# Kernel tuning notes

Hardware: AMD Instinct MI355X
Metric: run time of the kernel (lower is better)

The kernel has to match this reference:

```python
import jax, jax.numpy as jnp
import numpy as np

S, B, H, D, G = 2048, 2, 16, 128, 16  # seq, batch, heads, head_dim, v-quant groups


def setup_inputs() -> dict:
    key = jax.random.key(0)
    ks = jax.random.split(key, 9)
    # int8-valued activations stored as float (torch code does .to(torch.int8))
    q = jax.random.randint(ks[0], (S, B, H, D), -128, 128).astype(jnp.float32)
    k = jax.random.randint(ks[1], (S, B, H, D), -128, 128).astype(jnp.float32)
    v = jax.random.randint(ks[2], (S, B, H, D), -128, 128).astype(jnp.float32)
    qmin = jax.random.normal(ks[3], (S, B, H, 1), jnp.float32) * 0.01
    qscale = jax.random.uniform(ks[4], (S, B, H, 1), jnp.float32, 0.005, 0.02)
    kmin = jax.random.normal(ks[5], (S, B, H, 1), jnp.float32) * 0.01
    kscale = jax.random.uniform(ks[6], (S, B, H, 1), jnp.float32, 0.005, 0.02)
    vmin = jax.random.normal(ks[7], (G, B, H, D, 1), jnp.float32) * 0.01
    vscale = jax.random.uniform(ks[8], (G, B, H, D, 1), jnp.float32, 0.005, 0.02)
    return {"query_layer": q, "key_layer": k, "value_layer": v,
            "qmin": qmin, "qscale": qscale, "kmin": kmin, "kscale": kscale,
            "vmin": vmin, "vscale": vscale, "causal": 1}


def _attention(query_layer, key_layer, value_layer, qmin, qscale, kmin, kscale, vmin, vscale, causal):
    # s b h d -> b h s d ; emulate .to(torch.int8) (values are already int8-range ints)
    q = jnp.transpose(query_layer, (1, 2, 0, 3))
    k = jnp.transpose(key_layer, (1, 2, 0, 3))
    v = jnp.transpose(value_layer, (1, 2, 0, 3))
    # per-token quant factors: s b h 1 -> b h s 1
    qm = jnp.transpose(qmin[..., 0], (1, 2, 0))[..., None]
    qs = jnp.transpose(qscale[..., 0], (1, 2, 0))[..., None]
    km = jnp.transpose(kmin[..., 0], (1, 2, 0))[..., None]
    ksc = jnp.transpose(kscale[..., 0], (1, 2, 0))[..., None]
    # attnq_qk: dequantize per-token then QK^T
    qd = q * qs + qm
    kd = k * ksc + km
    scores = jnp.einsum('bhsd,bhtd->bhst', qd, kd)
    # softmaxq: scale by 1/sqrt(128), causal mask, softmax, int8 requant of probs
    scores = scores * jnp.float32(1.0 / np.sqrt(128.0))
    s = scores.shape[-1]
    if causal:
        mask = jnp.tril(jnp.ones((s, s), dtype=bool))
        scores = jnp.where(mask, scores, jnp.float32(-1e9))
    probs = jax.nn.softmax(scores, axis=-1)
    pmin = jnp.min(probs, axis=-1, keepdims=True)
    pmax = jnp.max(probs, axis=-1, keepdims=True)
    pscale = (pmax - pmin) / 255.0 + jnp.float32(1e-12)
    quant_prob = jnp.round((probs - pmin) / pscale)  # int8-range prob codes
    # attnq_pv: dequant probs (per query token) and V (per sequence group) then PV
    pd = quant_prob * pscale + pmin
    vm = jnp.transpose(vmin[..., 0], (1, 2, 0, 3))  # b h g d
    vs = jnp.transpose(vscale[..., 0], (1, 2, 0, 3))
    gs = v.shape[2] // vm.shape[2]  # group size along sequence
    vd = v * jnp.repeat(vs, gs, axis=2) + jnp.repeat(vm, gs, axis=2)
    out = jnp.einsum('bhst,bhtd->bhsd', pd, vd)
    b, h, sq, d = out.shape
    return jnp.transpose(out, (2, 0, 1, 3)).reshape(sq, b, h * d)  # s b (h d)


def reference(query_layer, key_layer, value_layer, qmin, qscale, kmin, kscale, vmin, vscale, causal):
    return _attention(query_layer, key_layer, value_layer, qmin, qscale, kmin, kscale, vmin, vscale, causal)
```

## Files before the change

kernel.cpp:

```cpp
#include <hip/hip_runtime.h>
#include <math.h>


#define S_LEN 2048
#define BATCH 2
#define NH    16
#define HD    128
#define RSTR  4096
#define SCALE2 (0.08838834764831845f * 1.4426950408889634f)
#define EXP2F(x) __builtin_amdgcn_exp2f(x)

typedef int v4i __attribute__((ext_vector_type(4)));
#define MFMA16(a,b,c) __builtin_amdgcn_mfma_i32_16x16x64_i8((a),(b),(c),0,0,0)

#define WS_K8   0u
#define WS_V8T  (8u*1024u*1024u)
#define WS_SK   (16u*1024u*1024u)
#define WS_GSV  (WS_SK + 256u*1024u)

__device__ __forceinline__ int sbsum(unsigned p) {
    return (int)(signed char)(p) + (int)(signed char)(p>>8)
         + (int)(signed char)(p>>16) + (int)(signed char)(p>>24);
}

__global__ __launch_bounds__(256) void prep_k(const float* __restrict__ K,
                                              signed char* __restrict__ K8,
                                              float* __restrict__ SKs)
{
    const int base = blockIdx.x*2048 + threadIdx.x;
    #pragma unroll
    for (int rep = 0; rep < 8; ++rep) {
        int idx = base + rep*256;
        float4 x = *(const float4*)(K + (size_t)idx*4);
        int a=(int)x.x, b=(int)x.y, c=(int)x.z, d=(int)x.w;
        ((int*)K8)[idx] = (a&255)|((b&255)<<8)|((c&255)<<16)|((d&255)<<24);
        float s = x.x + x.y + x.z + x.w;
        #pragma unroll
        for (int off = 16; off >= 1; off >>= 1) s += __shfl_xor(s, off);
        if ((threadIdx.x & 31) == 0) SKs[idx >> 5] = s;
    }
}

__global__ __launch_bounds__(256) void prep_v(const float* __restrict__ V,
                                              signed char* __restrict__ V8T,
                                              float* __restrict__ GSV)
{
    __shared__ int v8i[128*33];
    const int tid = threadIdx.x;
    const int bid = blockIdx.x;
    const int bh = bid & 31, ck = bid >> 5;
    const int b = bh >> 4, h = bh & 15;
    const int t0 = ck * 128;
    const int boff = b*2048 + h*128;
    #pragma unroll
    for (int it = 0; it < 16; ++it) {
        int idx = tid + it*256;
        int t = idx >> 5, dw = idx & 31;
        float4 x = *(const float4*)(V + (size_t)(t0+t)*RSTR + boff + 4*dw);
        int a=(int)x.x, b2=(int)x.y, c=(int)x.z, d=(int)x.w;
        v8i[t*33 + dw] = (a&255)|((b2&255)<<8)|((c&255)<<16)|((d&255)<<24);
    }
    __syncthreads();
    #pragma unroll
    for (int it = 0; it < 4; ++it) {
        int j = tid + it*256;
        int tg = j & 31, dw = j >> 5;
        unsigned r0 = (unsigned)v8i[(4*tg+0)*33 + dw];
        unsigned r1 = (unsigned)v8i[(4*tg+1)*33 + dw];
        unsigned r2 = (unsigned)v8i[(4*tg+2)*33 + dw];
        unsigned r3 = (unsigned)v8i[(4*tg+3)*33 + dw];
        unsigned x01 = __builtin_amdgcn_perm(r1, r0, 0x05010400u);
        unsigned x23 = __builtin_amdgcn_perm(r3, r2, 0x05010400u);
        unsigned y01 = __builtin_amdgcn_perm(r1, r0, 0x07030602u);
        unsigned y23 = __builtin_amdgcn_perm(r3, r2, 0x07030602u);
        unsigned p[4];
        p[0] = __builtin_amdgcn_perm(x23, x01, 0x05040100u);
        p[1] = __builtin_amdgcn_perm(x23, x01, 0x07060302u);
        p[2] = __builtin_amdgcn_perm(y23, y01, 0x05040100u);
        p[3] = __builtin_amdgcn_perm(y23, y01, 0x07060302u);
        int s[4];
        #pragma unroll
        for (int jj = 0; jj < 4; ++jj) {
            int d = 4*dw + jj;
            *(int*)(V8T + ((size_t)bh*128 + d)*2048 + t0 + 4*tg) = (int)p[jj];
            s[jj] = sbsum(p[jj]);
        }
        #pragma unroll
        for (int off = 1; off < 32; off <<= 1) {
            #pragma unroll
            for (int jj = 0; jj < 4; ++jj) s[jj] += __shfl_xor(s[jj], off);
        }
        if (tg == 0) {
            #pragma unroll
            for (int jj = 0; jj < 4; ++jj)
                GSV[((size_t)bh*16 + ck)*128 + 4*dw + jj] = (float)s[jj];
        }
    }
}

__global__ __launch_bounds__(256, 2) void attn_main(
    const float* __restrict__ Q,
    const signed char* __restrict__ K8, const signed char* __restrict__ V8T,
    const float* __restrict__ QMN, const float* __restrict__ QSC,
    const float* __restrict__ KMN, const float* __restrict__ KSC,
    const float* __restrict__ VMN, const float* __restrict__ VSC,
    const float* __restrict__ SKs, const float* __restrict__ GSV,
    const int* __restrict__ CAUSAL, float* __restrict__ OUT)
{
    __shared__ __align__(16) signed char q8s[64*144];
    __shared__ __align__(16) signed char k8s[128*144];
    __shared__ __align__(16) signed char v8s[128*144];
    __shared__ __align__(16) signed char pcs[64*144];
    __shared__ float rs_c1[64], rs_c2[64], rs_c3[64];
    __shared__ float rs_mx[64], rs_den[64], rs_mn[64];
    __shared__ float rs_u1[64], rs_w1[64], rs_psc[64], rs_pmn[64];
    __shared__ float ktA[128], ktB[128], ktC[128];
    __shared__ float vsA[128], vsB[128];
    __shared__ float vsumL[128], cgsL[128];

    const int tid  = threadIdx.x;
    const int w    = tid >> 6;
    const int lane = tid & 63;
    const int n    = lane & 15;
    const int quad = lane >> 4;
    const int bhi  = blockIdx.x & 31;
    const int qt   = 31 - (int)(blockIdx.x >> 5);
    const int b    = bhi >> 4, h = bhi & 15;
    const int causal = *CAUSAL;
    const int s0   = qt * 64;
    const int boff = b*2048 + h*128;
    const v4i vzero = {0,0,0,0};
    const v4i ones  = {0x01010101,0x01010101,0x01010101,0x01010101};

    #pragma unroll
    for (int it = 0; it < 8; ++it) {
        int idx = tid + it*256;
        int row = idx >> 5, d4 = (idx & 31) << 2;
        float4 x = *(const float4*)(Q + (size_t)(s0+row)*RSTR + boff + d4);
        int a=(int)x.x, b2=(int)x.y, c=(int)x.z, d=(int)x.w;
        *(int*)(q8s + row*144 + d4) = (a&255)|((b2&255)<<8)|((c&255)<<16)|((d&255)<<24);
    }
    if (tid < 64) {
        int si = (s0 + tid)*32 + bhi;
        rs_c1[tid] = QSC[si]; rs_c2[tid] = QMN[si];
    }
    __syncthreads();

    const int kt_end = causal ? ((s0 + 63) >> 7) : 15;

    v4i a0p = *(const v4i*)(q8s + (16*w + n)*144 + 16*quad);
    v4i a1p = *(const v4i*)(q8s + (16*w + n)*144 + 64 + 16*quad);

    {
        v4i qsum = MFMA16(a0p, ones, vzero);
        qsum = MFMA16(a1p, ones, qsum);
        if (n == 0) {
            #pragma unroll
            for (int r = 0; r < 4; ++r) {
                int qq = 16*w + 4*quad + r;
                rs_c3[qq] = fmaf(rs_c1[qq], (float)qsum[r], 128.0f*rs_c2[qq]);
            }
        }
    }
    __syncthreads();

    float c1r[4], c2r[4], c3r[4]; int qgr[4];
    #pragma unroll
    for (int r = 0; r < 4; ++r) {
        int qq = 16*w + 4*quad + r;
        c1r[r] = rs_c1[qq]; c2r[r] = rs_c2[qq]; c3r[r] = rs_c3[qq];
        qgr[r] = s0 + qq;
    }

    float m[4], l[4], mn[4];
    #pragma unroll
    for (int r = 0; r < 4; ++r) { m[r] = -INFINITY; l[r] = 0.f; mn[r] = INFINITY; }

#define P1_TILE(MASKED)                                                          \
  do {                                                                           \
    const int t0g = kt * 128;                                                    \
    __syncthreads();                                                             \
    _Pragma("unroll")                                                            \
    for (int it = 0; it < 4; ++it) {                                             \
        int idx = tid + it*256;                                                  \
        int trow = idx >> 3, doff = (idx & 7) << 4;                              \
        *(uint4*)(k8s + trow*144 + doff) =                                       \
            *(const uint4*)(K8 + ((size_t)(t0g+trow)*32 + bhi)*128 + doff);      \
    }                                                                            \
    if (tid < 128) {                                                             \
        int si = (t0g + tid)*32 + bhi;                                           \
        ktA[tid] = KSC[si]*SCALE2; ktB[tid] = KMN[si]*SCALE2; ktC[tid] = SKs[si];\
    }                                                                            \
    __syncthreads();                                                             \
    float tmax[4], sarr[8][4];                                                   \
    _Pragma("unroll")                                                            \
    for (int r = 0; r < 4; ++r) tmax[r] = -INFINITY;                             \
    _Pragma("unroll")                                                            \
    for (int tb = 0; tb < 8; ++tb) {                                             \
        v4i b0 = *(const v4i*)(k8s + (16*tb + n)*144 + 16*quad);                 \
        v4i b1 = *(const v4i*)(k8s + (16*tb + n)*144 + 64 + 16*quad);            \
        v4i acc = MFMA16(a0p, b0, vzero);                                        \
        acc = MFMA16(a1p, b1, acc);                                              \
        int tl = 16*tb + n;                                                      \
        float kA = ktA[tl], kB = ktB[tl], kC = ktC[tl];                          \
        _Pragma("unroll")                                                        \
        for (int r = 0; r < 4; ++r) {                                            \
            float Sf = (float)acc[r];                                            \
            float sv = fmaf(kA, fmaf(c1r[r], Sf, c2r[r]*kC), kB*c3r[r]);         \
            if (MASKED) sv = (t0g + tl > qgr[r]) ? -INFINITY : sv;               \
            sarr[tb][r] = sv;                                                    \
            tmax[r] = fmaxf(tmax[r], sv);                                        \
            mn[r] = fminf(mn[r], sv);                                            \
        }                                                                        \
    }                                                                            \
    _Pragma("unroll")                                                            \
    for (int r = 0; r < 4; ++r) {                                                \
        float mm = fmaxf(m[r], tmax[r]);                                         \
        if (mm > -INFINITY) {                                                    \
            float e0 = EXP2F(sarr[0][r]-mm) + EXP2F(sarr[1][r]-mm);              \
            float e1 = EXP2F(sarr[2][r]-mm) + EXP2F(sarr[3][r]-mm);              \
            float e2 = EXP2F(sarr[4][r]-mm) + EXP2F(sarr[5][r]-mm);              \
            float e3 = EXP2F(sarr[6][r]-mm) + EXP2F(sarr[7][r]-mm);              \
            l[r] = fmaf(l[r], EXP2F(m[r]-mm), (e0+e1)+(e2+e3));                  \
            m[r] = mm;                                                           \
        }                                                                        \
    }                                                                            \
  } while (0)

    {
        int kt;
        for (kt = 0; kt < kt_end; ++kt) P1_TILE(false);
        kt = kt_end;
        if (causal) P1_TILE(true); else P1_TILE(false);
    }

    #pragma unroll
    for (int r = 0; r < 4; ++r) {
        #pragma unroll
        for (int off = 1; off < 16; off <<= 1) {
            float m2 = __shfl_xor(m[r], off);
            float l2 = __shfl_xor(l[r], off);
            float n2 = __shfl_xor(mn[r], off);
            float mm = fmaxf(m[r], m2);
            if (mm > -INFINITY) l[r] = l[r]*EXP2F(m[r]-mm) + l2*EXP2F(m2-mm);
            m[r] = mm;
            mn[r] = fminf(mn[r], n2);
        }
        if (n == 0) {
            int qq = 16*w + 4*quad + r;
            rs_mx[qq] = m[r]; rs_den[qq] = l[r]; rs_mn[qq] = mn[r];
        }
    }
    __syncthreads();
    if (tid < 64) {
        float mx = rs_mx[tid], den = rs_den[tid], mnv = rs_mn[tid];
        float invd = 1.0f/den;
        int s = s0 + tid;
        bool hasmask = (causal != 0) && (s < S_LEN-1);
        float pmin = hasmask ? 0.0f : EXP2F(mnv - mx)*invd;
        float psc  = (invd - pmin)/255.0f + 1e-12f;
        float ipsc = 1.0f/psc;
        rs_u1[tid] = invd*ipsc; rs_w1[tid] = -pmin*ipsc;
        rs_psc[tid] = psc; rs_pmn[tid] = pmin;
    } else if (tid >= 128) {
        int d = tid - 128;
        float vsum = 0.f, cgs = 0.f;
        #pragma unroll
        for (int g = 0; g < 16; ++g) {
            float gs = GSV[((size_t)bhi*16 + g)*128 + d];
            int vi = ((g*BATCH + b)*NH + h)*HD + d;
            float vs = VSC[vi], vm = VMN[vi];
            vsum = fmaf(vs, gs, fmaf(128.0f, vm, vsum));
            if (g <= kt_end) cgs = fmaf(128.0f*vs, gs, fmaf(16384.0f, vm, cgs));
        }
        vsumL[d] = vsum; cgsL[d] = cgs;
    }
    __syncthreads();

    v4i qb0[4], qb1[4];
    float qc1[4], qc2[4], qc3[4], qmxn[4], qu1[4], qw1[4];
    int qgq[4];
    #pragma unroll
    for (int cb = 0; cb < 4; ++cb) {
        int qcol = 16*cb + n;
        qb0[cb] = *(const v4i*)(q8s + qcol*144 + 16*quad);
        qb1[cb] = *(const v4i*)(q8s + qcol*144 + 64 + 16*quad);
        qc1[cb] = rs_c1[qcol]; qc2[cb] = rs_c2[qcol]; qc3[cb] = rs_c3[qcol];
        qmxn[cb] = -rs_mx[qcol]; qu1[cb] = rs_u1[qcol]; qw1[cb] = rs_w1[qcol];
        qgq[cb] = s0 + qcol;
    }

    float outa[4][8];
    #pragma unroll
    for (int r = 0; r < 4; ++r)
        #pragma unroll
        for (int db = 0; db < 8; ++db) outa[r][db] = 0.f;

#define P2_TILE(MASKED)                                                          \
  do {                                                                           \
    const int t0g = kt * 128;                                                    \
    __syncthreads();                      \
    _Pragma("unroll")                                                            \
    for (int it = 0; it < 4; ++it) {                                             \
        int idx = tid + it*256;                                                  \
        int trow = idx >> 3, doff = (idx & 7) << 4;                              \
        *(uint4*)(v8s + trow*144 + doff) =                                       \
            *(const uint4*)(V8T + ((size_t)bhi*128 + trow)*2048 + t0g + doff);   \
    }                                                                            \
    if (tid < 128) {                                                             \
        int si = (t0g + tid)*32 + bhi;                                           \
        ktA[tid] = KSC[si]*SCALE2; ktB[tid] = KMN[si]*SCALE2; ktC[tid] = SKs[si];\
    } else {                                                                     \
        int d = tid - 128;                                                       \
        int vi = ((kt*BATCH + b)*NH + h)*HD + d;                                 \
        vsA[d] = VSC[vi]; vsB[d] = VMN[vi];                                      \
    }                                                                            \
    __syncthreads();                                                             \
    _Pragma("unroll")                                                            \
    for (int rb = 0; rb < 2; ++rb) {                                             \
        int trow = 32*w + 16*rb;                                                 \
        const signed char* kp = K8 + ((size_t)(t0g+trow+n)*32 + bhi)*128         \
                                   + 16*quad;                                    \
        v4i a0 = *(const v4i*)kp;              \
        v4i a1 = *(const v4i*)(kp + 64);                                         \
        float ksr[4], kmr[4], skr[4];                                            \
        int tgb = t0g + trow + 4*quad;                                           \
        _Pragma("unroll")                                                        \
        for (int r = 0; r < 4; ++r) {                                            \
            int tl = trow + 4*quad + r;                                          \
            ksr[r] = ktA[tl]; kmr[r] = ktB[tl]; skr[r] = ktC[tl];                \
        }                                                                        \
        _Pragma("unroll")                                                        \
        for (int cb = 0; cb < 4; ++cb) {                                         \
            v4i acc = MFMA16(a0, qb0[cb], vzero);                                \
            acc = MFMA16(a1, qb1[cb], acc);                                      \
            int cby[4];                                                          \
            _Pragma("unroll")                                                    \
            for (int r = 0; r < 4; ++r) {                                        \
                float Sf = (float)acc[r];                                        \
                float x = fmaf(ksr[r], fmaf(qc1[cb], Sf, qc2[cb]*skr[r]),        \
                               fmaf(kmr[r], qc3[cb], qmxn[cb]));                 \
                if (MASKED) x = (tgb + r > qgq[cb]) ? -INFINITY : x;             \
                float e = EXP2F(x);                                              \
                float f = fmaf(e, qu1[cb], qw1[cb]) + 8388608.0f;   \
                cby[r] = __float_as_int(f);                                      \
            }                                                                    \
            unsigned t01 = __builtin_amdgcn_perm((unsigned)cby[1],               \
                                                 (unsigned)cby[0], 0x00000400u); \
            unsigned t23 = __builtin_amdgcn_perm((unsigned)cby[3],               \
                                                 (unsigned)cby[2], 0x04000000u); \
            int packed = (int)(__builtin_amdgcn_perm(t23, t01, 0x07060100u)      \
                               ^ 0x80808080u);          \
            *(int*)(pcs + (16*cb + n)*144 + trow + 4*quad) = packed;             \
        }                                                                        \
    }                                                                            \
    __syncthreads();                                                             \
    {                                                                            \
        v4i a0 = *(const v4i*)(pcs + (16*w + n)*144 + 16*quad);                  \
        v4i a1 = *(const v4i*)(pcs + (16*w + n)*144 + 64 + 16*quad);             \
        v4i c1a = MFMA16(a0, ones, vzero);                                       \
        c1a = MFMA16(a1, ones, c1a);                                             \
        float c1f[4];                                                            \
        _Pragma("unroll")                                                        \
        for (int r = 0; r < 4; ++r) c1f[r] = (float)c1a[r];                      \
        _Pragma("unroll")                                                        \
        for (int db = 0; db < 8; ++db) {                                         \
            v4i b0 = *(const v4i*)(v8s + (16*db + n)*144 + 16*quad);             \
            v4i b1 = *(const v4i*)(v8s + (16*db + n)*144 + 64 + 16*quad);        \
            v4i cv = MFMA16(a0, b0, vzero);                                      \
            cv = MFMA16(a1, b1, cv);                                             \
            int d = 16*db + n;                                                   \
            float vs = vsA[d], vm = vsB[d];                                      \
            _Pragma("unroll")                                                    \
            for (int r = 0; r < 4; ++r)                                          \
                outa[r][db] = fmaf(vs, (float)cv[r],                             \
                                   fmaf(vm, c1f[r], outa[r][db]));               \
        }                                                                        \
    }                                                                            \
  } while (0)

    {
        int kt;
        for (kt = 0; kt < kt_end; ++kt) P2_TILE(false);
        kt = kt_end;
        if (causal) P2_TILE(true); else P2_TILE(false);
    }

    float pscr[4], pmnr[4];
    #pragma unroll
    for (int r = 0; r < 4; ++r) {
        int qq = 16*w + 4*quad + r;
        pscr[r] = rs_psc[qq]; pmnr[r] = rs_pmn[qq];
    }
    #pragma unroll
    for (int db = 0; db < 8; ++db) {
        int d = 16*db + n;
        float vsum = vsumL[d];
        float cgs  = cgsL[d];
        #pragma unroll
        for (int r = 0; r < 4; ++r) {
            int s = s0 + 16*w + 4*quad + r;
            OUT[(size_t)s*RSTR + boff + d] = fmaf(pscr[r], outa[r][db] + cgs, pmnr[r]*vsum);
        }
    }
}

extern "C" void kernel_launch(void* const* d_in, const int* in_sizes, int n_in,
                              void* d_out, int out_size, void* d_ws, size_t ws_size,
                              hipStream_t stream) {
    (void)in_sizes; (void)n_in; (void)out_size; (void)ws_size;
    const float* Q   = (const float*)d_in[0];
    const float* K   = (const float*)d_in[1];
    const float* V   = (const float*)d_in[2];
    const float* QMN = (const float*)d_in[3];
    const float* QSC = (const float*)d_in[4];
    const float* KMN = (const float*)d_in[5];
    const float* KSC = (const float*)d_in[6];
    const float* VMN = (const float*)d_in[7];
    const float* VSC = (const float*)d_in[8];
    const int*   CS  = (const int*)d_in[9];
    float* out = (float*)d_out;

    char* ws = (char*)d_ws;
    signed char* K8  = (signed char*)(ws + WS_K8);
    signed char* V8T = (signed char*)(ws + WS_V8T);
    float* SKs  = (float*)(ws + WS_SK);
    float* GSVp = (float*)(ws + WS_GSV);

    prep_v<<<512, 256, 0, stream>>>(V, V8T, GSVp);
    prep_k<<<1024, 256, 0, stream>>>(K, K8, SKs);
    attn_main<<<1024, 256, 0, stream>>>(Q, K8, V8T, QMN, QSC, KMN, KSC, VMN, VSC,
                                        SKs, GSVp, CS, out);
}
```

Measured before the change: 243.3 us.

## Split two-pass attention kernel into separate stats and output kernels

The single attention kernel, which ran a softmax-statistics pass and then an output pass, is split into two kernels. The first kernel writes per-row max, denominator and min to workspace. The second reads them back, recomputes the Q row sums, and reloads Q fragments from LDS inside the loop instead of keeping them in registers. Each kernel uses less LDS and fewer registers, so launch bounds rise to 4 and 3 blocks per CU, at the cost of an extra launch, repeated Q loading and conversion, and a global round trip for the statistics.

```diff
diff --git a/kernel.cpp b/kernel.cpp
--- a/kernel.cpp
+++ b/kernel.cpp
@@ -16,7 +16,10 @@
 #define WS_K8   0u
 #define WS_V8T  (8u*1024u*1024u)
 #define WS_SK   (16u*1024u*1024u)
-#define WS_GSV  (WS_SK + 256u*1024u)
+#define WS_GSV  (WS_SK  + 256u*1024u)
+#define WS_STMX (WS_GSV + 256u*1024u)
+#define WS_STDN (WS_STMX + 256u*1024u)
+#define WS_STMN (WS_STDN + 256u*1024u)
 
 __device__ __forceinline__ int sbsum(unsigned p) {
     return (int)(signed char)(p) + (int)(signed char)(p>>8)
@@ -98,25 +101,17 @@
     }
 }
 
-__global__ __launch_bounds__(256, 2) void attn_main(
-    const float* __restrict__ Q,
-    const signed char* __restrict__ K8, const signed char* __restrict__ V8T,
+__global__ __launch_bounds__(256, 4) void attn_p1(
+    const float* __restrict__ Q, const signed char* __restrict__ K8,
     const float* __restrict__ QMN, const float* __restrict__ QSC,
     const float* __restrict__ KMN, const float* __restrict__ KSC,
-    const float* __restrict__ VMN, const float* __restrict__ VSC,
-    const float* __restrict__ SKs, const float* __restrict__ GSV,
-    const int* __restrict__ CAUSAL, float* __restrict__ OUT)
+    const float* __restrict__ SKs, const int* __restrict__ CAUSAL,
+    float* __restrict__ STmx, float* __restrict__ STden, float* __restrict__ STmn)
 {
     __shared__ __align__(16) signed char q8s[64*144];
     __shared__ __align__(16) signed char k8s[128*144];
-    __shared__ __align__(16) signed char v8s[128*144];
-    __shared__ __align__(16) signed char pcs[64*144];
     __shared__ float rs_c1[64], rs_c2[64], rs_c3[64];
-    __shared__ float rs_mx[64], rs_den[64], rs_mn[64];
-    __shared__ float rs_u1[64], rs_w1[64], rs_psc[64], rs_pmn[64];
     __shared__ float ktA[128], ktB[128], ktC[128];
-    __shared__ float vsA[128], vsB[128];
-    __shared__ float vsumL[128], cgsL[128];
 
     const int tid  = threadIdx.x;
     const int w    = tid >> 6;
@@ -125,10 +120,9 @@
     const int quad = lane >> 4;
     const int bhi  = blockIdx.x & 31;
     const int qt   = 31 - (int)(blockIdx.x >> 5);
-    const int b    = bhi >> 4, h = bhi & 15;
     const int causal = *CAUSAL;
     const int s0   = qt * 64;
-    const int boff = b*2048 + h*128;
+    const int boff = (bhi >> 4)*2048 + (bhi & 15)*128;
     const v4i vzero = {0,0,0,0};
     const v4i ones  = {0x01010101,0x01010101,0x01010101,0x01010101};
 
@@ -248,43 +242,107 @@
         }
         if (n == 0) {
             int qq = 16*w + 4*quad + r;
-            rs_mx[qq] = m[r]; rs_den[qq] = l[r]; rs_mn[qq] = mn[r];
-        }
+            int gi = (int)blockIdx.x*64 + qq;
+            STmx[gi] = m[r]; STden[gi] = l[r]; STmn[gi] = mn[r];
+        }
+    }
+}
+
+__global__ __launch_bounds__(256, 3) void attn_p2(
+    const float* __restrict__ Q,
+    const signed char* __restrict__ K8, const signed char* __restrict__ V8T,
+    const float* __restrict__ QMN, const float* __restrict__ QSC,
+    const float* __restrict__ KMN, const float* __restrict__ KSC,
+    const float* __restrict__ VMN, const float* __restrict__ VSC,
+    const float* __restrict__ SKs, const float* __restrict__ GSV,
+    const float* __restrict__ STmx, const float* __restrict__ STden,
+    const float* __restrict__ STmn,
+    const int* __restrict__ CAUSAL, float* __restrict__ OUT)
+{
+    __shared__ __align__(16) signed char q8s[64*144];
+    __shared__ __align__(16) signed char v8s[128*144];
+    __shared__ __align__(16) signed char pcs[64*144];
+    __shared__ float rs_c1[64], rs_c2[64], rs_c3[64];
+    __shared__ float rs_mx[64], rs_u1[64], rs_w1[64], rs_psc[64], rs_pmn[64];
+    __shared__ float ktA[128], ktB[128], ktC[128];
+    __shared__ float vsA[128], vsB[128];
+    __shared__ float vsumL[128], cgsL[128];
+
+    const int tid  = threadIdx.x;
+    const int w    = tid >> 6;
+    const int lane = tid & 63;
+    const int n    = lane & 15;
+    const int quad = lane >> 4;
+    const int bhi  = blockIdx.x & 31;
+    const int qt   = 31 - (int)(blockIdx.x >> 5);
+    const int b    = bhi >> 4, h = bhi & 15;
+    const int causal = *CAUSAL;
+    const int s0   = qt * 64;
+    const int boff = b*2048 + h*128;
+    const v4i vzero = {0,0,0,0};
+    const v4i ones  = {0x01010101,0x01010101,0x01010101,0x01010101};
+
+    const int kt_end = causal ? ((s0 + 63) >> 7) : 15;
+
+    #pragma unroll
+    for (int it = 0; it < 8; ++it) {
+        int idx = tid + it*256;
+        int row = idx >> 5, d4 = (idx & 31) << 2;
+        float4 x = *(const float4*)(Q + (size_t)(s0+row)*RSTR + boff + d4);
+        int a=(int)x.x, b2=(int)x.y, c=(int)x.z, d=(int)x.w;
+        *(int*)(q8s + row*144 + d4) = (a&255)|((b2&255)<<8)|((c&255)<<16)|((d&255)<<24);
+    }
+    if (tid < 64) {
+        int si = (s0 + tid)*32 + bhi;
+        rs_c1[tid] = QSC[si]; rs_c2[tid] = QMN[si];
+    } else if (tid >= 128) {
+        int d = tid - 128;
+        float vsum = 0.f, cgs = 0.f;
+        #pragma unroll
+        for (int g = 0; g < 16; ++g) {
+            float gs = GSV[((size_t)bhi*16 + g)*128 + d];
+            int vi = ((g*BATCH + b)*NH + h)*HD + d;
+            float vs = VSC[vi], vm = VMN[vi];
+            vsum = fmaf(vs, gs, fmaf(128.0f, vm, vsum));
+            if (g <= kt_end) cgs = fmaf(128.0f*vs, gs, fmaf(16384.0f, vm, cgs));
+        }
+        vsumL[d] = vsum; cgsL[d] = cgs;
     }
     __syncthreads();
+
+    {
+        v4i a0p = *(const v4i*)(q8s + (16*w + n)*144 + 16*quad);
+        v4i a1p = *(const v4i*)(q8s + (16*w + n)*144 + 64 + 16*quad);
+        v4i qsum = MFMA16(a0p, ones, vzero);
+        qsum = MFMA16(a1p, ones, qsum);
+        if (n == 0) {
+            #pragma unroll
+            for (int r = 0; r < 4; ++r) {
+                int qq = 16*w + 4*quad + r;
+                rs_c3[qq] = fmaf(rs_c1[qq], (float)qsum[r], 128.0f*rs_c2[qq]);
+            }
+        }
+    }
     if (tid < 64) {
-        float mx = rs_mx[tid], den = rs_den[tid], mnv = rs_mn[tid];
+        int gi = (int)blockIdx.x*64 + tid;
+        float mx = STmx[gi], den = STden[gi], mnv = STmn[gi];
         float invd = 1.0f/den;
         int s = s0 + tid;
         bool hasmask = (causal != 0) && (s < S_LEN-1);
         float pmin = hasmask ? 0.0f : EXP2F(mnv - mx)*invd;
         float psc  = (invd - pmin)/255.0f + 1e-12f;
         float ipsc = 1.0f/psc;
+        rs_mx[tid] = mx;
         rs_u1[tid] = invd*ipsc; rs_w1[tid] = -pmin*ipsc;
         rs_psc[tid] = psc; rs_pmn[tid] = pmin;
-    } else if (tid >= 128) {
-        int d = tid - 128;
-        float vsum = 0.f, cgs = 0.f;
-        #pragma unroll
-        for (int g = 0; g < 16; ++g) {
-            float gs = GSV[((size_t)bhi*16 + g)*128 + d];
-            int vi = ((g*BATCH + b)*NH + h)*HD + d;
-            float vs = VSC[vi], vm = VMN[vi];
-            vsum = fmaf(vs, gs, fmaf(128.0f, vm, vsum));
-            if (g <= kt_end) cgs = fmaf(128.0f*vs, gs, fmaf(16384.0f, vm, cgs));
-        }
-        vsumL[d] = vsum; cgsL[d] = cgs;
     }
     __syncthreads();
 
-    v4i qb0[4], qb1[4];
     float qc1[4], qc2[4], qc3[4], qmxn[4], qu1[4], qw1[4];
     int qgq[4];
     #pragma unroll
     for (int cb = 0; cb < 4; ++cb) {
         int qcol = 16*cb + n;
-        qb0[cb] = *(const v4i*)(q8s + qcol*144 + 16*quad);
-        qb1[cb] = *(const v4i*)(q8s + qcol*144 + 64 + 16*quad);
         qc1[cb] = rs_c1[qcol]; qc2[cb] = rs_c2[qcol]; qc3[cb] = rs_c3[qcol];
         qmxn[cb] = -rs_mx[qcol]; qu1[cb] = rs_u1[qcol]; qw1[cb] = rs_w1[qcol];
         qgq[cb] = s0 + qcol;
@@ -332,8 +390,10 @@
         }                                                                        \
         _Pragma("unroll")                                                        \
         for (int cb = 0; cb < 4; ++cb) {                                         \
-            v4i acc = MFMA16(a0, qb0[cb], vzero);                                \
-            acc = MFMA16(a1, qb1[cb], acc);                                      \
+            v4i qb0 = *(const v4i*)(q8s + (16*cb + n)*144 + 16*quad);            \
+            v4i qb1 = *(const v4i*)(q8s + (16*cb + n)*144 + 64 + 16*quad);       \
+            v4i acc = MFMA16(a0, qb0, vzero);                                    \
+            acc = MFMA16(a1, qb1, acc);                                          \
             int cby[4];                                                          \
             _Pragma("unroll")                                                    \
             for (int r = 0; r < 4; ++r) {                                        \
@@ -426,9 +486,14 @@
     signed char* V8T = (signed char*)(ws + WS_V8T);
     float* SKs  = (float*)(ws + WS_SK);
     float* GSVp = (float*)(ws + WS_GSV);
-
+    float* STmx = (float*)(ws + WS_STMX);
+    float* STdn = (float*)(ws + WS_STDN);
+    float* STmn = (float*)(ws + WS_STMN);
+
+    prep_k<<<1024, 256, 0, stream>>>(K, K8, SKs);
     prep_v<<<512, 256, 0, stream>>>(V, V8T, GSVp);
-    prep_k<<<1024, 256, 0, stream>>>(K, K8, SKs);
-    attn_main<<<1024, 256, 0, stream>>>(Q, K8, V8T, QMN, QSC, KMN, KSC, VMN, VSC,
-                                        SKs, GSVp, CS, out);
-}
+    attn_p1<<<1024, 256, 0, stream>>>(Q, K8, QMN, QSC, KMN, KSC, SKs, CS,
+                                      STmx, STdn, STmn);
+    attn_p2<<<1024, 256, 0, stream>>>(Q, K8, V8T, QMN, QSC, KMN, KSC, VMN, VSC,
+                                      SKs, GSVp, STmx, STdn, STmn, CS, out);
+}
```

New measurement: 257.4 us. 5.8% more time.

## Double-buffer K tiles in pass one, merge prep kernels, skip unneeded min tracking

Applied to the files above, without the earlier changes.

Pass one now prefetches the next K tile and its scale factors into registers while MFMAs run on the current tile, then writes them into a second LDS buffer, so each tile needs one barrier instead of two. The K double buffer is carved out of LDS shared with the V and prob buffers, so total shared memory stays about the same. The two prep kernels become one launch that branches on block index. Row-min tracking is skipped for causal tiles that are not the last query tile, since masked entries make the min fixed there. The costs are extra register pressure from the prefetch and more complicated control flow.

```diff
diff --git a/kernel.cpp b/kernel.cpp
--- a/kernel.cpp
+++ b/kernel.cpp
@@ -23,77 +23,76 @@
          + (int)(signed char)(p>>16) + (int)(signed char)(p>>24);
 }
 
-__global__ __launch_bounds__(256) void prep_k(const float* __restrict__ K,
-                                              signed char* __restrict__ K8,
-                                              float* __restrict__ SKs)
-{
-    const int base = blockIdx.x*2048 + threadIdx.x;
-    #pragma unroll
-    for (int rep = 0; rep < 8; ++rep) {
-        int idx = base + rep*256;
-        float4 x = *(const float4*)(K + (size_t)idx*4);
-        int a=(int)x.x, b=(int)x.y, c=(int)x.z, d=(int)x.w;
-        ((int*)K8)[idx] = (a&255)|((b&255)<<8)|((c&255)<<16)|((d&255)<<24);
-        float s = x.x + x.y + x.z + x.w;
-        #pragma unroll
-        for (int off = 16; off >= 1; off >>= 1) s += __shfl_xor(s, off);
-        if ((threadIdx.x & 31) == 0) SKs[idx >> 5] = s;
-    }
-}
-
-__global__ __launch_bounds__(256) void prep_v(const float* __restrict__ V,
-                                              signed char* __restrict__ V8T,
-                                              float* __restrict__ GSV)
+__global__ __launch_bounds__(256) void prep(
+    const float* __restrict__ K, const float* __restrict__ V,
+    signed char* __restrict__ K8, float* __restrict__ SKs,
+    signed char* __restrict__ V8T, float* __restrict__ GSV)
 {
     __shared__ int v8i[128*33];
     const int tid = threadIdx.x;
-    const int bid = blockIdx.x;
-    const int bh = bid & 31, ck = bid >> 5;
-    const int b = bh >> 4, h = bh & 15;
-    const int t0 = ck * 128;
-    const int boff = b*2048 + h*128;
-    #pragma unroll
-    for (int it = 0; it < 16; ++it) {
-        int idx = tid + it*256;
-        int t = idx >> 5, dw = idx & 31;
-        float4 x = *(const float4*)(V + (size_t)(t0+t)*RSTR + boff + 4*dw);
-        int a=(int)x.x, b2=(int)x.y, c=(int)x.z, d=(int)x.w;
-        v8i[t*33 + dw] = (a&255)|((b2&255)<<8)|((c&255)<<16)|((d&255)<<24);
-    }
-    __syncthreads();
-    #pragma unroll
-    for (int it = 0; it < 4; ++it) {
-        int j = tid + it*256;
-        int tg = j & 31, dw = j >> 5;
-        unsigned r0 = (unsigned)v8i[(4*tg+0)*33 + dw];
-        unsigned r1 = (unsigned)v8i[(4*tg+1)*33 + dw];
-        unsigned r2 = (unsigned)v8i[(4*tg+2)*33 + dw];
-        unsigned r3 = (unsigned)v8i[(4*tg+3)*33 + dw];
-        unsigned x01 = __builtin_amdgcn_perm(r1, r0, 0x05010400u);
-        unsigned x23 = __builtin_amdgcn_perm(r3, r2, 0x05010400u);
-        unsigned y01 = __builtin_amdgcn_perm(r1, r0, 0x07030602u);
-        unsigned y23 = __builtin_amdgcn_perm(r3, r2, 0x07030602u);
-        unsigned p[4];
-        p[0] = __builtin_amdgcn_perm(x23, x01, 0x05040100u);
-        p[1] = __builtin_amdgcn_perm(x23, x01, 0x07060302u);
-        p[2] = __builtin_amdgcn_perm(y23, y01, 0x05040100u);
-        p[3] = __builtin_amdgcn_perm(y23, y01, 0x07060302u);
-        int s[4];
-        #pragma unroll
-        for (int jj = 0; jj < 4; ++jj) {
-            int d = 4*dw + jj;
-            *(int*)(V8T + ((size_t)bh*128 + d)*2048 + t0 + 4*tg) = (int)p[jj];
-            s[jj] = sbsum(p[jj]);
-        }
-        #pragma unroll
-        for (int off = 1; off < 32; off <<= 1) {
+    const int bx  = blockIdx.x;
+    if (bx >= 512) {
+        const int base = (bx - 512)*2048 + tid;
+        #pragma unroll
+        for (int rep = 0; rep < 8; ++rep) {
+            int idx = base + rep*256;
+            float4 x = *(const float4*)(K + (size_t)idx*4);
+            int a=(int)x.x, b=(int)x.y, c=(int)x.z, d=(int)x.w;
+            ((int*)K8)[idx] = (a&255)|((b&255)<<8)|((c&255)<<16)|((d&255)<<24);
+            float s = x.x + x.y + x.z + x.w;
             #pragma unroll
-            for (int jj = 0; jj < 4; ++jj) s[jj] += __shfl_xor(s[jj], off);
-        }
-        if (tg == 0) {
+            for (int off = 16; off >= 1; off >>= 1) s += __shfl_xor(s, off);
+            if ((tid & 31) == 0) SKs[idx >> 5] = s;
+        }
+    } else {
+        const int bid = bx;
+        const int bh = bid & 31, ck = bid >> 5;
+        const int b = bh >> 4, h = bh & 15;
+        const int t0 = ck * 128;
+        const int boff = b*2048 + h*128;
+        #pragma unroll
+        for (int it = 0; it < 16; ++it) {
+            int idx = tid + it*256;
+            int t = idx >> 5, dw = idx & 31;
+            float4 x = *(const float4*)(V + (size_t)(t0+t)*RSTR + boff + 4*dw);
+            int a=(int)x.x, b2=(int)x.y, c=(int)x.z, d=(int)x.w;
+            v8i[t*33 + dw] = (a&255)|((b2&255)<<8)|((c&255)<<16)|((d&255)<<24);
+        }
+        __syncthreads();
+        #pragma unroll
+        for (int it = 0; it < 4; ++it) {
+            int j = tid + it*256;
+            int tg = j & 31, dw = j >> 5;
+            unsigned r0 = (unsigned)v8i[(4*tg+0)*33 + dw];
+            unsigned r1 = (unsigned)v8i[(4*tg+1)*33 + dw];
+            unsigned r2 = (unsigned)v8i[(4*tg+2)*33 + dw];
+            unsigned r3 = (unsigned)v8i[(4*tg+3)*33 + dw];
+            unsigned x01 = __builtin_amdgcn_perm(r1, r0, 0x05010400u);
+            unsigned x23 = __builtin_amdgcn_perm(r3, r2, 0x05010400u);
+            unsigned y01 = __builtin_amdgcn_perm(r1, r0, 0x07030602u);
+            unsigned y23 = __builtin_amdgcn_perm(r3, r2, 0x07030602u);
+            unsigned p[4];
+            p[0] = __builtin_amdgcn_perm(x23, x01, 0x05040100u);
+            p[1] = __builtin_amdgcn_perm(x23, x01, 0x07060302u);
+            p[2] = __builtin_amdgcn_perm(y23, y01, 0x05040100u);
+            p[3] = __builtin_amdgcn_perm(y23, y01, 0x07060302u);
+            int s[4];
             #pragma unroll
-            for (int jj = 0; jj < 4; ++jj)
-                GSV[((size_t)bh*16 + ck)*128 + 4*dw + jj] = (float)s[jj];
+            for (int jj = 0; jj < 4; ++jj) {
+                int d = 4*dw + jj;
+                *(int*)(V8T + ((size_t)bh*128 + d)*2048 + t0 + 4*tg) = (int)p[jj];
+                s[jj] = sbsum(p[jj]);
+            }
+            #pragma unroll
+            for (int off = 1; off < 32; off <<= 1) {
+                #pragma unroll
+                for (int jj = 0; jj < 4; ++jj) s[jj] += __shfl_xor(s[jj], off);
+            }
+            if (tg == 0) {
+                #pragma unroll
+                for (int jj = 0; jj < 4; ++jj)
+                    GSV[((size_t)bh*16 + ck)*128 + 4*dw + jj] = (float)s[jj];
+            }
         }
     }
 }
@@ -108,15 +107,16 @@
     const int* __restrict__ CAUSAL, float* __restrict__ OUT)
 {
     __shared__ __align__(16) signed char q8s[64*144];
-    __shared__ __align__(16) signed char k8s[128*144];
-    __shared__ __align__(16) signed char v8s[128*144];
-    __shared__ __align__(16) signed char pcs[64*144];
+    __shared__ __align__(16) signed char un[2*128*144];
     __shared__ float rs_c1[64], rs_c2[64], rs_c3[64];
     __shared__ float rs_mx[64], rs_den[64], rs_mn[64];
     __shared__ float rs_u1[64], rs_w1[64], rs_psc[64], rs_pmn[64];
-    __shared__ float ktA[128], ktB[128], ktC[128];
+    __shared__ float ktA[2][128], ktB[2][128], ktC[2][128];
     __shared__ float vsA[128], vsB[128];
     __shared__ float vsumL[128], cgsL[128];
+
+    signed char* v8s = un;
+    signed char* pcs = un + 128*144;
 
     const int tid  = threadIdx.x;
     const int w    = tid >> 6;
@@ -132,6 +132,8 @@
     const v4i vzero = {0,0,0,0};
     const v4i ones  = {0x01010101,0x01010101,0x01010101,0x01010101};
 
+    const int kt_end = causal ? ((s0 + 63) >> 7) : 15;
+
     #pragma unroll
     for (int it = 0; it < 8; ++it) {
         int idx = tid + it*256;
@@ -140,13 +142,22 @@
         int a=(int)x.x, b2=(int)x.y, c=(int)x.z, d=(int)x.w;
         *(int*)(q8s + row*144 + d4) = (a&255)|((b2&255)<<8)|((c&255)<<16)|((d&255)<<24);
     }
+    #pragma unroll
+    for (int it = 0; it < 4; ++it) {
+        int idx = tid + it*256;
+        int trow = idx >> 3, doff = (idx & 7) << 4;
+        *(uint4*)(un + trow*144 + doff) =
+            *(const uint4*)(K8 + ((size_t)trow*32 + bhi)*128 + doff);
+    }
     if (tid < 64) {
         int si = (s0 + tid)*32 + bhi;
         rs_c1[tid] = QSC[si]; rs_c2[tid] = QMN[si];
+    } else if (tid >= 128) {
+        int d = tid - 128;
+        int si = d*32 + bhi;
+        ktA[0][d] = KSC[si]*SCALE2; ktB[0][d] = KMN[si]*SCALE2; ktC[0][d] = SKs[si];
     }
     __syncthreads();
-
-    const int kt_end = causal ? ((s0 + 63) >> 7) : 15;
 
     v4i a0p = *(const v4i*)(q8s + (16*w + n)*144 + 16*quad);
     v4i a1p = *(const v4i*)(q8s + (16*w + n)*144 + 64 + 16*quad);
@@ -176,33 +187,38 @@
     #pragma unroll
     for (int r = 0; r < 4; ++r) { m[r] = -INFINITY; l[r] = 0.f; mn[r] = INFINITY; }
 
-#define P1_TILE(MASKED)                                                          \
+#define P1_TILE(MASKED, DOMN)                                                    \
   do {                                                                           \
     const int t0g = kt * 128;                                                    \
-    __syncthreads();                                                             \
-    _Pragma("unroll")                                                            \
-    for (int it = 0; it < 4; ++it) {                                             \
-        int idx = tid + it*256;                                                  \
-        int trow = idx >> 3, doff = (idx & 7) << 4;                              \
-        *(uint4*)(k8s + trow*144 + doff) =                                       \
-            *(const uint4*)(K8 + ((size_t)(t0g+trow)*32 + bhi)*128 + doff);      \
-    }                                                                            \
-    if (tid < 128) {                                                             \
-        int si = (t0g + tid)*32 + bhi;                                           \
-        ktA[tid] = KSC[si]*SCALE2; ktB[tid] = KMN[si]*SCALE2; ktC[tid] = SKs[si];\
-    }                                                                            \
-    __syncthreads();                                                             \
+    const int cur = kt & 1;                                                      \
+    const signed char* k8c = un + cur*(128*144);                                 \
+    signed char* k8n = un + (cur^1)*(128*144);                                   \
+    const bool hn = kt < kt_end;                                                 \
+    uint4 nx[4]; float nA = 0.f, nB = 0.f, nC = 0.f;                             \
+    if (hn) {                                                                    \
+        _Pragma("unroll")                                                        \
+        for (int it = 0; it < 4; ++it) {                                         \
+            int idx = tid + it*256;                                              \
+            int trow = idx >> 3, doff = (idx & 7) << 4;                          \
+            nx[it] = *(const uint4*)(K8 +                                        \
+                      ((size_t)(t0g + 128 + trow)*32 + bhi)*128 + doff);         \
+        }                                                                        \
+        if (tid < 128) {                                                         \
+            int si = (t0g + 128 + tid)*32 + bhi;                                 \
+            nA = KSC[si]*SCALE2; nB = KMN[si]*SCALE2; nC = SKs[si];              \
+        }                                                                        \
+    }                                                                            \
     float tmax[4], sarr[8][4];                                                   \
     _Pragma("unroll")                                                            \
     for (int r = 0; r < 4; ++r) tmax[r] = -INFINITY;                             \
     _Pragma("unroll")                                                            \
     for (int tb = 0; tb < 8; ++tb) {                                             \
-        v4i b0 = *(const v4i*)(k8s + (16*tb + n)*144 + 16*quad);                 \
-        v4i b1 = *(const v4i*)(k8s + (16*tb + n)*144 + 64 + 16*quad);            \
+        v4i b0 = *(const v4i*)(k8c + (16*tb + n)*144 + 16*quad);                 \
+        v4i b1 = *(const v4i*)(k8c + (16*tb + n)*144 + 64 + 16*quad);            \
         v4i acc = MFMA16(a0p, b0, vzero);                                        \
         acc = MFMA16(a1p, b1, acc);                                              \
         int tl = 16*tb + n;                                                      \
-        float kA = ktA[tl], kB = ktB[tl], kC = ktC[tl];                          \
+        float kA = ktA[cur][tl], kB = ktB[cur][tl], kC = ktC[cur][tl];           \
         _Pragma("unroll")                                                        \
         for (int r = 0; r < 4; ++r) {                                            \
             float Sf = (float)acc[r];                                            \
@@ -210,7 +226,7 @@
             if (MASKED) sv = (t0g + tl > qgr[r]) ? -INFINITY : sv;               \
             sarr[tb][r] = sv;                                                    \
             tmax[r] = fmaxf(tmax[r], sv);                                        \
-            mn[r] = fminf(mn[r], sv);                                            \
+            if (DOMN) mn[r] = fminf(mn[r], sv);                                  \
         }                                                                        \
     }                                                                            \
     _Pragma("unroll")                                                            \
@@ -225,13 +241,30 @@
             m[r] = mm;                                                           \
         }                                                                        \
     }                                                                            \
+    if (hn) {                                                                    \
+        _Pragma("unroll")                                                        \
+        for (int it = 0; it < 4; ++it) {                                         \
+            int idx = tid + it*256;                                              \
+            int trow = idx >> 3, doff = (idx & 7) << 4;                          \
+            *(uint4*)(k8n + trow*144 + doff) = nx[it];                           \
+        }                                                                        \
+        if (tid < 128) {                                                         \
+            ktA[cur^1][tid] = nA; ktB[cur^1][tid] = nB; ktC[cur^1][tid] = nC;    \
+        }                                                                        \
+    }                                                                            \
+    __syncthreads();                                                             \
   } while (0)
 
-    {
+    if ((!causal) || (qt == 31)) {
         int kt;
-        for (kt = 0; kt < kt_end; ++kt) P1_TILE(false);
+        for (kt = 0; kt < kt_end; ++kt) P1_TILE(false, true);
         kt = kt_end;
-        if (causal) P1_TILE(true); else P1_TILE(false);
+        if (causal) P1_TILE(true, true); else P1_TILE(false, true);
+    } else {
+        int kt;
+        for (kt = 0; kt < kt_end; ++kt) P1_TILE(false, false);
+        kt = kt_end;
+        P1_TILE(true, false);
     }
 
     #pragma unroll
@@ -309,7 +342,8 @@
     }                                                                            \
     if (tid < 128) {                                                             \
         int si = (t0g + tid)*32 + bhi;                                           \
-        ktA[tid] = KSC[si]*SCALE2; ktB[tid] = KMN[si]*SCALE2; ktC[tid] = SKs[si];\
+        ktA[0][tid] = KSC[si]*SCALE2; ktB[0][tid] = KMN[si]*SCALE2;              \
+        ktC[0][tid] = SKs[si];                                                   \
     } else {                                                                     \
         int d = tid - 128;                                                       \
         int vi = ((kt*BATCH + b)*NH + h)*HD + d;                                 \
@@ -328,7 +362,7 @@
         _Pragma("unroll")                                                        \
         for (int r = 0; r < 4; ++r) {                                            \
             int tl = trow + 4*quad + r;                                          \
-            ksr[r] = ktA[tl]; kmr[r] = ktB[tl]; skr[r] = ktC[tl];                \
+            ksr[r] = ktA[0][tl]; kmr[r] = ktB[0][tl]; skr[r] = ktC[0][tl];       \
         }                                                                        \
         _Pragma("unroll")                                                        \
         for (int cb = 0; cb < 4; ++cb) {                                         \
@@ -427,8 +461,7 @@
     float* SKs  = (float*)(ws + WS_SK);
     float* GSVp = (float*)(ws + WS_GSV);
 
-    prep_v<<<512, 256, 0, stream>>>(V, V8T, GSVp);
-    prep_k<<<1024, 256, 0, stream>>>(K, K8, SKs);
+    prep<<<1536, 256, 0, stream>>>(K, V, K8, SKs, V8T, GSVp);
     attn_main<<<1024, 256, 0, stream>>>(Q, K8, V8T, QMN, QSC, KMN, KSC, VMN, VSC,
                                         SKs, GSVp, CS, out);
 }
```

New measurement: 244.8 us. No clear change (+0.6%).
